# Performance work log

Hardware: AMD Instinct MI355X
Metric: run time of the kernel (lower is better)

The kernel has to match this reference:

```python
import jax, jax.numpy as jnp
import numpy as np

NEG_INF = -1e30

def setup_inputs() -> dict:
    key = jax.random.key(0)
    kC, kQ, kw = jax.random.split(key, 3)
    B, D, Lc, Lq = 32, 128, 2048, 64
    C = jax.random.normal(kC, (B, D, Lc), dtype=jnp.float32)
    Q = jax.random.normal(kQ, (B, D, Lq), dtype=jnp.float32)
    qmask = jnp.ones((B, Lq), dtype=jnp.float32)
    # trilinear weight, uniform(-sqrt(1/D), sqrt(1/D)) as in the torch init
    lim = (1.0 / D) ** 0.5
    w = jax.random.uniform(kw, (3 * D,), dtype=jnp.float32, minval=-lim, maxval=lim)
    return {"C": C, "Q": Q, "qmask": qmask, "w": w}

def reference(C, Q, qmask, w):
    # C: (B, D, Lc), Q: (B, D, Lq), qmask: (B, Lq), w: (3D,)
    Ct = jnp.transpose(C, (0, 2, 1))  # (B, Lc, D)
    Qt = jnp.transpose(Q, (0, 2, 1))  # (B, Lq, D)
    D = Ct.shape[-1]
    w1, w2, w3 = w[:D], w[D:2 * D], w[2 * D:]
    # trilinear similarity S[b,i,j] = Ct[b,i].w1 + Qt[b,j].w2 + (Ct[b,i]*Qt[b,j]).w3
    # computed WITHOUT the (B,Lc,Lq,3D) intermediate
    sc = Ct @ w1                                   # (B, Lc)
    sq = Qt @ w2                                   # (B, Lq)
    scq = jnp.einsum('bid,bjd->bij', Ct * w3, Qt)  # (B, Lc, Lq)
    S = sc[:, :, None] + sq[None if False else slice(None), None, :] + scq  # (B, Lc, Lq)
    m = qmask[:, None, :]                          # (B, 1, Lq)
    S1 = jax.nn.softmax(S * m + (1.0 - m) * NEG_INF, axis=2)  # over query axis
    S2 = jax.nn.softmax(S, axis=1)                             # over context axis
    A = jnp.einsum('bij,bjd->bid', S1, Qt)                     # (B, Lc, D)
    S1S2T = jnp.einsum('bij,bkj->bik', S1, S2)                 # (B, Lc, Lc) via S1 @ S2^T
    Bm = jnp.einsum('bik,bkd->bid', S1S2T, Ct)                 # (B, Lc, D)
    out = jnp.concatenate([Ct, A, Ct * A, Ct * Bm], axis=2)    # (B, Lc, 4D)
    # dropout is identity in eval mode
    return jnp.transpose(out, (0, 2, 1))                       # (B, 4D, Lc)
```

## Files before the change

### kernel.cpp

```cpp
#include <hip/hip_runtime.h>

#define LC 2048
#define DD 128
#define LQ 64
#define NPART 32
#define PADA 136
#define PADC 72

typedef unsigned short u16;
typedef unsigned int u32;
typedef __attribute__((ext_vector_type(8))) short bf16x8;
typedef __attribute__((ext_vector_type(4))) float f32x4;

__device__ inline u16 f2b(float f) {
  u32 u = __float_as_uint(f);
  u32 r = (u + 0x7fffu + ((u >> 16) & 1u)) >> 16;
  return (u16)r;
}
__device__ inline float b2f(u16 u) { return __uint_as_float(((u32)u) << 16); }
__device__ inline u32 pack2(float a, float b) {
  return (u32)f2b(a) | ((u32)f2b(b) << 16);
}

__global__ __launch_bounds__(256) void k13(const float* __restrict__ C,
                                           const float* __restrict__ Q,
                                           const float* __restrict__ w,
                                           const float* __restrict__ qmask,
                                           u16* __restrict__ S1g,
                                           float* __restrict__ Tu_part,
                                           float* __restrict__ Z_part, int B) {
  __shared__ u16 ldsA[128 * PADC];
  __shared__ u16 ldsB[64 * PADA];
  __shared__ float scp4[4][64], sqp4[4][64];
  __shared__ float scL[64], sqs[64], mkS[64], invL[64];
  int b = blockIdx.y, bx = blockIdx.x;
  int i0 = bx * 64, t = threadIdx.x;
  const float* Cb = C + (size_t)b * DD * LC;
  const float* Qb = Q + (size_t)b * DD * LQ;
  if (t < 64) mkS[t] = qmask[b * LQ + t];
  {
    int i = t & 63, dg = t >> 6;
    const float* Cp = Cb + i0 + i;
    float scp = 0.f;
#pragma unroll
    for (int dp = 0; dp < 16; ++dp) {
      int d = dg * 32 + 2 * dp;
      float c0 = Cp[(size_t)d * LC];
      float c1 = Cp[(size_t)(d + 1) * LC];
      scp = fmaf(c0, w[d], fmaf(c1, w[d + 1], scp));
      *(u32*)&ldsA[i * PADA + d] = pack2(c0, c1);
    }
    scp4[dg][i] = scp;
  }
  {
    int j = t & 63, dg = t >> 6;
    const float* Qp = Qb + j;
    float sqp = 0.f;
#pragma unroll
    for (int dp = 0; dp < 16; ++dp) {
      int d = dg * 32 + 2 * dp;
      float q0 = Qp[(size_t)d * LQ];
      float q1 = Qp[(size_t)(d + 1) * LQ];
      sqp = fmaf(q0, w[DD + d], fmaf(q1, w[DD + d + 1], sqp));
      *(u32*)&ldsB[j * PADA + d] = pack2(q0 * w[2 * DD + d], q1 * w[2 * DD + d + 1]);
    }
    sqp4[dg][j] = sqp;
  }
  __syncthreads();
  if (t < 64) scL[t] = scp4[0][t] + scp4[1][t] + scp4[2][t] + scp4[3][t];
  else if (t < 128) {
    int j = t - 64;
    sqs[j] = sqp4[0][j] + sqp4[1][j] + sqp4[2][j] + sqp4[3][j];
  }
  int lane = t & 63, wv = t >> 6;
  int lr = lane & 15, kg = lane >> 4;
  f32x4 acc[4];
#pragma unroll
  for (int nt = 0; nt < 4; ++nt) acc[nt] = (f32x4){0.f, 0.f, 0.f, 0.f};
#pragma unroll
  for (int ks = 0; ks < 4; ++ks) {
    bf16x8 af = *(bf16x8*)&ldsA[(wv * 16 + lr) * PADA + ks * 32 + kg * 8];
    bf16x8 bf[4];
#pragma unroll
    for (int nt = 0; nt < 4; ++nt)
      bf[nt] = *(bf16x8*)&ldsB[(nt * 16 + lr) * PADA + ks * 32 + kg * 8];
#pragma unroll
    for (int nt = 0; nt < 4; ++nt)
      acc[nt] = __builtin_amdgcn_mfma_f32_16x16x32_bf16(af, bf[nt], acc[nt], 0, 0, 0);
  }
  __syncthreads();
  {
    int ib = wv * 16 + kg * 4;
    float ev[4][4];
    float ps[4] = {0.f, 0.f, 0.f, 0.f};
#pragma unroll
    for (int nt = 0; nt < 4; ++nt) {
      int j = nt * 16 + lr;
      float sqv = sqs[j], mkv = mkS[j];
#pragma unroll
      for (int r = 0; r < 4; ++r) {
        float e = __expf(acc[nt][r] + scL[ib + r] + sqv);
        ev[nt][r] = e;
        ps[r] = fmaf(mkv, e, ps[r]);
      }
    }
#pragma unroll
    for (int r = 0; r < 4; ++r) {
      ps[r] += __shfl_xor(ps[r], 1, 64);
      ps[r] += __shfl_xor(ps[r], 2, 64);
      ps[r] += __shfl_xor(ps[r], 4, 64);
      ps[r] += __shfl_xor(ps[r], 8, 64);
    }
#pragma unroll
    for (int nt = 0; nt < 4; ++nt) {
      int j = nt * 16 + lr;
      u32 pk[2] = {pack2(ev[nt][0], ev[nt][1]), pack2(ev[nt][2], ev[nt][3])};
      *(uint2*)&ldsB[j * PADC + ib] = *(uint2*)pk;
    }
    if (lr == 0) {
#pragma unroll
      for (int r = 0; r < 4; ++r) invL[ib + r] = 1.f / fmaxf(ps[r], 1e-30f);
    }
  }
  {
    int d = t >> 1, half = t & 1;
    const float* src = Cb + (size_t)d * LC + i0 + half * 32;
#pragma unroll
    for (int ip = 0; ip < 8; ++ip) {
      float4 v = *(const float4*)&src[ip * 4];
      u32 pk[2] = {pack2(v.x, v.y), pack2(v.z, v.w)};
      *(uint2*)&ldsA[d * PADC + half * 32 + ip * 4] = *(uint2*)pk;
    }
  }
  __syncthreads();
  if (t < 64) {
    const u32* row = (const u32*)&ldsB[t * PADC];
    float z = 0.f;
#pragma unroll
    for (int q = 0; q < 32; ++q) {
      u32 v = row[q];
      z += b2f((u16)v) + b2f((u16)(v >> 16));
    }
    Z_part[((size_t)bx * B + b) * LQ + t] = z;
  }
  {
    int i = t >> 2, q4 = t & 3;
    float inv = invL[i];
    u32 opk[8];
#pragma unroll
    for (int q = 0; q < 8; ++q) {
      int j = q4 * 16 + 2 * q;
      float a0 = b2f(ldsB[j * PADC + i]) * mkS[j] * inv;
      float a1 = b2f(ldsB[(j + 1) * PADC + i]) * mkS[j + 1] * inv;
      opk[q] = pack2(a0, a1);
    }
    u16* dst = S1g + ((size_t)b * LC + i0 + i) * LQ + q4 * 16;
    *(uint4*)&dst[0] = *(uint4*)&opk[0];
    *(uint4*)&dst[8] = *(uint4*)&opk[4];
  }
  f32x4 tacc[2][4];
#pragma unroll
  for (int mt = 0; mt < 2; ++mt)
#pragma unroll
    for (int nt = 0; nt < 4; ++nt) tacc[mt][nt] = (f32x4){0.f, 0.f, 0.f, 0.f};
#pragma unroll
  for (int ks = 0; ks < 2; ++ks) {
    bf16x8 af[2], bf[4];
#pragma unroll
    for (int mt = 0; mt < 2; ++mt)
      af[mt] = *(bf16x8*)&ldsA[((wv * 2 + mt) * 16 + lr) * PADC + ks * 32 + kg * 8];
#pragma unroll
    for (int nt = 0; nt < 4; ++nt)
      bf[nt] = *(bf16x8*)&ldsB[(nt * 16 + lr) * PADC + ks * 32 + kg * 8];
#pragma unroll
    for (int mt = 0; mt < 2; ++mt)
#pragma unroll
      for (int nt = 0; nt < 4; ++nt)
        tacc[mt][nt] = __builtin_amdgcn_mfma_f32_16x16x32_bf16(af[mt], bf[nt],
                                                               tacc[mt][nt], 0, 0, 0);
  }
  float* Tp = Tu_part + ((size_t)bx * B + b) * LQ * DD;
#pragma unroll
  for (int mt = 0; mt < 2; ++mt)
#pragma unroll
    for (int nt = 0; nt < 4; ++nt) {
      int j = nt * 16 + lr;
      int db = (wv * 2 + mt) * 16 + kg * 4;
      *(f32x4*)&Tp[(size_t)j * DD + db] = tacc[mt][nt];
    }
}

__global__ __launch_bounds__(256) void k3b(const float* __restrict__ Tu_part,
                                           const float* __restrict__ Z_part,
                                           const float* __restrict__ Q,
                                           u16* __restrict__ TzT,
                                           u16* __restrict__ Qbf, int B) {
  __shared__ float Tsm[16][68];
  __shared__ float ziL[64];
  int b = blockIdx.y, d0 = blockIdx.x * 16;
  int t = threadIdx.x;
  {
    int dq = d0 + (t >> 4), jq = (t & 15) * 4;
    const float* qp = Q + ((size_t)b * DD + dq) * LQ + jq;
    u32 pk[2] = {pack2(qp[0], qp[1]), pack2(qp[2], qp[3])};
    *(uint2*)&Qbf[((size_t)b * DD + dq) * LQ + jq] = *(uint2*)pk;
  }
  int dd = t & 15, jg = t >> 4;
  float acc[4] = {};
#pragma unroll
  for (int p = 0; p < NPART; ++p) {
    const float* src = Tu_part + ((size_t)p * B + b) * LQ * DD + d0 + dd;
#pragma unroll
    for (int jj = 0; jj < 4; ++jj) acc[jj] += src[(jg * 4 + jj) * DD];
  }
  if (t < 64) {
    float z = 0.f;
#pragma unroll
    for (int p = 0; p < NPART; ++p) z += Z_part[((size_t)p * B + b) * LQ + t];
    ziL[t] = 1.f / z;
  }
  *(float4*)&Tsm[dd][jg * 4] = make_float4(acc[0], acc[1], acc[2], acc[3]);
  __syncthreads();
  if (t < 128) {
    int d = t >> 3, seg = t & 7;
    u32 pk[4];
#pragma unroll
    for (int q = 0; q < 4; ++q) {
      int j = seg * 8 + q * 2;
      pk[q] = pack2(Tsm[d][j] * ziL[j], Tsm[d][j + 1] * ziL[j + 1]);
    }
    *(uint4*)&TzT[((size_t)b * DD + d0 + d) * LQ + seg * 8] = *(uint4*)pk;
  }
}

__global__ __launch_bounds__(256) void k4(const u16* __restrict__ S1g,
                                          const u16* __restrict__ Qbf,
                                          const u16* __restrict__ TzT,
                                          const float* __restrict__ C,
                                          float* __restrict__ out) {
  int b = blockIdx.y, i0 = blockIdx.x * 64, t = threadIdx.x;
  int lane = t & 63, wv = t >> 6;
  int lr = lane & 15, kg = lane >> 4;
  bf16x8 Af[2];
  {
    size_t ri = ((size_t)b * LC + i0 + wv * 16 + lr) * LQ;
    Af[0] = *(const bf16x8*)&S1g[ri + kg * 8];
    Af[1] = *(const bf16x8*)&S1g[ri + 32 + kg * 8];
  }
  const u16* Qb = Qbf + (size_t)b * DD * LQ;
  const u16* Tzb = TzT + (size_t)b * DD * LQ;
  const float* Cb = C + (size_t)b * DD * LC + i0;
  float* outb = out + (size_t)b * 4 * DD * LC + i0;
  int irow = wv * 16 + kg * 4;
#pragma unroll
  for (int nt = 0; nt < 8; ++nt) {
    int d = nt * 16 + lr;
    bf16x8 QB[2], TB[2];
#pragma unroll
    for (int ks = 0; ks < 2; ++ks) {
      QB[ks] = *(const bf16x8*)&Qb[(size_t)d * LQ + ks * 32 + kg * 8];
      TB[ks] = *(const bf16x8*)&Tzb[(size_t)d * LQ + ks * 32 + kg * 8];
    }
    f32x4 accA = {0.f, 0.f, 0.f, 0.f}, accB = {0.f, 0.f, 0.f, 0.f};
    accA = __builtin_amdgcn_mfma_f32_16x16x32_bf16(Af[0], QB[0], accA, 0, 0, 0);
    accA = __builtin_amdgcn_mfma_f32_16x16x32_bf16(Af[1], QB[1], accA, 0, 0, 0);
    accB = __builtin_amdgcn_mfma_f32_16x16x32_bf16(Af[0], TB[0], accB, 0, 0, 0);
    accB = __builtin_amdgcn_mfma_f32_16x16x32_bf16(Af[1], TB[1], accB, 0, 0, 0);
    float4 c4 = *(const float4*)&Cb[(size_t)d * LC + irow];
    float4 oA = make_float4(accA[0], accA[1], accA[2], accA[3]);
    float4 oCA = make_float4(c4.x * accA[0], c4.y * accA[1], c4.z * accA[2],
                             c4.w * accA[3]);
    float4 oCB = make_float4(c4.x * accB[0], c4.y * accB[1], c4.z * accB[2],
                             c4.w * accB[3]);
    *(float4*)&outb[(size_t)d * LC + irow] = c4;
    *(float4*)&outb[(size_t)(DD + d) * LC + irow] = oA;
    *(float4*)&outb[(size_t)(2 * DD + d) * LC + irow] = oCA;
    *(float4*)&outb[(size_t)(3 * DD + d) * LC + irow] = oCB;
  }
}

extern "C" void kernel_launch(void* const* d_in, const int* in_sizes, int n_in,
                              void* d_out, int out_size, void* d_ws, size_t ws_size,
                              hipStream_t stream) {
  const float* C = (const float*)d_in[0];
  const float* Q = (const float*)d_in[1];
  const float* qmask = (const float*)d_in[2];
  const float* w = (const float*)d_in[3];
  float* out = (float*)d_out;
  int B = in_sizes[2] / LQ;

  char* p = (char*)d_ws;
  u16* S1g = (u16*)p;           p += (size_t)B * LC * LQ * 2;
  u16* TzT = (u16*)p;           p += (size_t)B * DD * LQ * 2;
  u16* Qbf = (u16*)p;           p += (size_t)B * DD * LQ * 2;
  float* Tu_part = (float*)p;   p += (size_t)NPART * B * LQ * DD * 4;
  float* Z_part = (float*)p;

  k13<<<dim3(LC / 64, B), 256, 0, stream>>>(C, Q, w, qmask, S1g, Tu_part, Z_part, B);
  k3b<<<dim3(DD / 16, B), 256, 0, stream>>>(Tu_part, Z_part, Q, TzT, Qbf, B);
  k4<<<dim3(LC / 64, B), 256, 0, stream>>>(S1g, Qbf, TzT, C, out);
}
```

Baseline: 77.70 us.

## Precompute weighted bf16 Q once per batch in a new prologue kernel

```diff
diff --git a/kernel.cpp b/kernel.cpp
--- a/kernel.cpp
+++ b/kernel.cpp
@@ -4,8 +4,6 @@
 #define DD 128
 #define LQ 64
 #define NPART 32
-#define PADA 136
-#define PADC 72
 
 typedef unsigned short u16;
 typedef unsigned int u32;
@@ -22,56 +20,102 @@
   return (u32)f2b(a) | ((u32)f2b(b) << 16);
 }
 
+__global__ __launch_bounds__(256) void kq(const float* __restrict__ Q,
+                                          const float* __restrict__ w,
+                                          u16* __restrict__ Qwg,
+                                          float* __restrict__ sqg,
+                                          u16* __restrict__ Qbf) {
+  __shared__ float qs[128][65];
+  __shared__ float red[4][64];
+  int b = blockIdx.x, t = threadIdx.x;
+  const float* Qb = Q + (size_t)b * DD * LQ;
+  {
+    int base = t * 32;
+#pragma unroll
+    for (int q = 0; q < 8; ++q) {
+      float4 v = *(const float4*)&Qb[base + q * 4];
+      int k = base + q * 4;
+      int d = k >> 6, j = k & 63;
+      qs[d][j] = v.x; qs[d][j + 1] = v.y; qs[d][j + 2] = v.z; qs[d][j + 3] = v.w;
+    }
+  }
+  __syncthreads();
+  {
+    int j = t & 63, dq = t >> 6;
+    float sqp = 0.f;
+    u32 pk[16];
+#pragma unroll
+    for (int dp = 0; dp < 16; ++dp) {
+      int d = dq * 32 + 2 * dp;
+      float q0 = qs[d][j], q1 = qs[d + 1][j];
+      sqp = fmaf(q0, w[DD + d], fmaf(q1, w[DD + d + 1], sqp));
+      pk[dp] = pack2(q0 * w[2 * DD + d], q1 * w[2 * DD + d + 1]);
+    }
+    u16* dst = Qwg + ((size_t)b * LQ + j) * DD + dq * 32;
+#pragma unroll
+    for (int q = 0; q < 4; ++q) *(uint4*)&dst[q * 8] = *(uint4*)&pk[q * 4];
+    red[dq][j] = sqp;
+  }
+  {
+    int d = t >> 1, half = t & 1;
+    u32 pk[16];
+#pragma unroll
+    for (int q = 0; q < 16; ++q)
+      pk[q] = pack2(qs[d][half * 32 + 2 * q], qs[d][half * 32 + 2 * q + 1]);
+    u16* dst = Qbf + ((size_t)b * DD + d) * LQ + half * 32;
+#pragma unroll
+    for (int q = 0; q < 4; ++q) *(uint4*)&dst[q * 8] = *(uint4*)&pk[q * 4];
+  }
+  __syncthreads();
+  if (t < 64) sqg[b * LQ + t] = red[0][t] + red[1][t] + red[2][t] + red[3][t];
+}
+
 __global__ __launch_bounds__(256) void k13(const float* __restrict__ C,
-                                           const float* __restrict__ Q,
+                                           const u16* __restrict__ Qwg,
+                                           const float* __restrict__ sqg,
+                                           const float* __restrict__ qmask,
                                            const float* __restrict__ w,
-                                           const float* __restrict__ qmask,
                                            u16* __restrict__ S1g,
                                            float* __restrict__ Tu_part,
                                            float* __restrict__ Z_part, int B) {
-  __shared__ u16 ldsA[128 * PADC];
-  __shared__ u16 ldsB[64 * PADA];
-  __shared__ float scp4[4][64], sqp4[4][64];
+  __shared__ u16 ldsA[128 * 72];
+  __shared__ u16 ldsB[64 * 136];
+  __shared__ float scp4[4][64];
   __shared__ float scL[64], sqs[64], mkS[64], invL[64];
   int b = blockIdx.y, bx = blockIdx.x;
   int i0 = bx * 64, t = threadIdx.x;
   const float* Cb = C + (size_t)b * DD * LC;
-  const float* Qb = Q + (size_t)b * DD * LQ;
-  if (t < 64) mkS[t] = qmask[b * LQ + t];
   {
     int i = t & 63, dg = t >> 6;
     const float* Cp = Cb + i0 + i;
     float scp = 0.f;
+    u32 pk[16];
 #pragma unroll
     for (int dp = 0; dp < 16; ++dp) {
       int d = dg * 32 + 2 * dp;
       float c0 = Cp[(size_t)d * LC];
       float c1 = Cp[(size_t)(d + 1) * LC];
       scp = fmaf(c0, w[d], fmaf(c1, w[d + 1], scp));
-      *(u32*)&ldsA[i * PADA + d] = pack2(c0, c1);
-    }
+      pk[dp] = pack2(c0, c1);
+    }
+#pragma unroll
+    for (int q = 0; q < 4; ++q)
+      *(uint4*)&ldsA[i * 136 + dg * 32 + q * 8] = *(uint4*)&pk[q * 4];
     scp4[dg][i] = scp;
   }
   {
-    int j = t & 63, dg = t >> 6;
-    const float* Qp = Qb + j;
-    float sqp = 0.f;
-#pragma unroll
-    for (int dp = 0; dp < 16; ++dp) {
-      int d = dg * 32 + 2 * dp;
-      float q0 = Qp[(size_t)d * LQ];
-      float q1 = Qp[(size_t)(d + 1) * LQ];
-      sqp = fmaf(q0, w[DD + d], fmaf(q1, w[DD + d + 1], sqp));
-      *(u32*)&ldsB[j * PADA + d] = pack2(q0 * w[2 * DD + d], q1 * w[2 * DD + d + 1]);
-    }
-    sqp4[dg][j] = sqp;
+    int row = t & 63, quarter = t >> 6;
+    const u16* src = Qwg + ((size_t)b * LQ + row) * DD + quarter * 32;
+#pragma unroll
+    for (int q = 0; q < 4; ++q)
+      *(uint4*)&ldsB[row * 136 + quarter * 32 + q * 8] = *(const uint4*)&src[q * 8];
+  }
+  if (t < 64) {
+    sqs[t] = sqg[b * LQ + t];
+    mkS[t] = qmask[b * LQ + t];
   }
   __syncthreads();
   if (t < 64) scL[t] = scp4[0][t] + scp4[1][t] + scp4[2][t] + scp4[3][t];
-  else if (t < 128) {
-    int j = t - 64;
-    sqs[j] = sqp4[0][j] + sqp4[1][j] + sqp4[2][j] + sqp4[3][j];
-  }
   int lane = t & 63, wv = t >> 6;
   int lr = lane & 15, kg = lane >> 4;
   f32x4 acc[4];
@@ -79,11 +123,11 @@
   for (int nt = 0; nt < 4; ++nt) acc[nt] = (f32x4){0.f, 0.f, 0.f, 0.f};
 #pragma unroll
   for (int ks = 0; ks < 4; ++ks) {
-    bf16x8 af = *(bf16x8*)&ldsA[(wv * 16 + lr) * PADA + ks * 32 + kg * 8];
+    bf16x8 af = *(bf16x8*)&ldsA[(wv * 16 + lr) * 136 + ks * 32 + kg * 8];
     bf16x8 bf[4];
 #pragma unroll
     for (int nt = 0; nt < 4; ++nt)
-      bf[nt] = *(bf16x8*)&ldsB[(nt * 16 + lr) * PADA + ks * 32 + kg * 8];
+      bf[nt] = *(bf16x8*)&ldsB[(nt * 16 + lr) * 136 + ks * 32 + kg * 8];
 #pragma unroll
     for (int nt = 0; nt < 4; ++nt)
       acc[nt] = __builtin_amdgcn_mfma_f32_16x16x32_bf16(af, bf[nt], acc[nt], 0, 0, 0);
@@ -115,7 +159,7 @@
     for (int nt = 0; nt < 4; ++nt) {
       int j = nt * 16 + lr;
       u32 pk[2] = {pack2(ev[nt][0], ev[nt][1]), pack2(ev[nt][2], ev[nt][3])};
-      *(uint2*)&ldsB[j * PADC + ib] = *(uint2*)pk;
+      *(uint2*)&ldsB[j * 72 + ib] = *(uint2*)pk;
     }
     if (lr == 0) {
 #pragma unroll
@@ -125,16 +169,20 @@
   {
     int d = t >> 1, half = t & 1;
     const float* src = Cb + (size_t)d * LC + i0 + half * 32;
+    u32 pk[16];
 #pragma unroll
     for (int ip = 0; ip < 8; ++ip) {
       float4 v = *(const float4*)&src[ip * 4];
-      u32 pk[2] = {pack2(v.x, v.y), pack2(v.z, v.w)};
-      *(uint2*)&ldsA[d * PADC + half * 32 + ip * 4] = *(uint2*)pk;
-    }
+      pk[2 * ip] = pack2(v.x, v.y);
+      pk[2 * ip + 1] = pack2(v.z, v.w);
+    }
+#pragma unroll
+    for (int q = 0; q < 4; ++q)
+      *(uint4*)&ldsA[d * 72 + half * 32 + q * 8] = *(uint4*)&pk[q * 4];
   }
   __syncthreads();
   if (t < 64) {
-    const u32* row = (const u32*)&ldsB[t * PADC];
+    const u32* row = (const u32*)&ldsB[t * 72];
     float z = 0.f;
 #pragma unroll
     for (int q = 0; q < 32; ++q) {
@@ -150,8 +198,8 @@
 #pragma unroll
     for (int q = 0; q < 8; ++q) {
       int j = q4 * 16 + 2 * q;
-      float a0 = b2f(ldsB[j * PADC + i]) * mkS[j] * inv;
-      float a1 = b2f(ldsB[(j + 1) * PADC + i]) * mkS[j + 1] * inv;
+      float a0 = b2f(ldsB[j * 72 + i]) * mkS[j] * inv;
+      float a1 = b2f(ldsB[(j + 1) * 72 + i]) * mkS[j + 1] * inv;
       opk[q] = pack2(a0, a1);
     }
     u16* dst = S1g + ((size_t)b * LC + i0 + i) * LQ + q4 * 16;
@@ -168,10 +216,10 @@
     bf16x8 af[2], bf[4];
 #pragma unroll
     for (int mt = 0; mt < 2; ++mt)
-      af[mt] = *(bf16x8*)&ldsA[((wv * 2 + mt) * 16 + lr) * PADC + ks * 32 + kg * 8];
+      af[mt] = *(bf16x8*)&ldsA[((wv * 2 + mt) * 16 + lr) * 72 + ks * 32 + kg * 8];
 #pragma unroll
     for (int nt = 0; nt < 4; ++nt)
-      bf[nt] = *(bf16x8*)&ldsB[(nt * 16 + lr) * PADC + ks * 32 + kg * 8];
+      bf[nt] = *(bf16x8*)&ldsB[(nt * 16 + lr) * 72 + ks * 32 + kg * 8];
 #pragma unroll
     for (int mt = 0; mt < 2; ++mt)
 #pragma unroll
@@ -192,26 +240,19 @@
 
 __global__ __launch_bounds__(256) void k3b(const float* __restrict__ Tu_part,
                                            const float* __restrict__ Z_part,
-                                           const float* __restrict__ Q,
-                                           u16* __restrict__ TzT,
-                                           u16* __restrict__ Qbf, int B) {
+                                           u16* __restrict__ TzT, int B) {
   __shared__ float Tsm[16][68];
   __shared__ float ziL[64];
   int b = blockIdx.y, d0 = blockIdx.x * 16;
   int t = threadIdx.x;
   {
-    int dq = d0 + (t >> 4), jq = (t & 15) * 4;
-    const float* qp = Q + ((size_t)b * DD + dq) * LQ + jq;
-    u32 pk[2] = {pack2(qp[0], qp[1]), pack2(qp[2], qp[3])};
-    *(uint2*)&Qbf[((size_t)b * DD + dq) * LQ + jq] = *(uint2*)pk;
-  }
-  int dd = t & 15, jg = t >> 4;
-  float acc[4] = {};
-#pragma unroll
-  for (int p = 0; p < NPART; ++p) {
-    const float* src = Tu_part + ((size_t)p * B + b) * LQ * DD + d0 + dd;
-#pragma unroll
-    for (int jj = 0; jj < 4; ++jj) acc[jj] += src[(jg * 4 + jj) * DD];
+    int j = t >> 2, dseg = t & 3;
+    f32x4 acc = {0.f, 0.f, 0.f, 0.f};
+#pragma unroll
+    for (int p = 0; p < NPART; ++p)
+      acc += *(const f32x4*)&Tu_part[((size_t)p * B + b) * LQ * DD + (size_t)j * DD + d0 + dseg * 4];
+#pragma unroll
+    for (int r = 0; r < 4; ++r) Tsm[dseg * 4 + r][j] = acc[r];
   }
   if (t < 64) {
     float z = 0.f;
@@ -219,7 +260,6 @@
     for (int p = 0; p < NPART; ++p) z += Z_part[((size_t)p * B + b) * LQ + t];
     ziL[t] = 1.f / z;
   }
-  *(float4*)&Tsm[dd][jg * 4] = make_float4(acc[0], acc[1], acc[2], acc[3]);
   __syncthreads();
   if (t < 128) {
     int d = t >> 3, seg = t & 7;
@@ -293,10 +333,13 @@
   u16* S1g = (u16*)p;           p += (size_t)B * LC * LQ * 2;
   u16* TzT = (u16*)p;           p += (size_t)B * DD * LQ * 2;
   u16* Qbf = (u16*)p;           p += (size_t)B * DD * LQ * 2;
+  u16* Qwg = (u16*)p;           p += (size_t)B * LQ * DD * 2;
   float* Tu_part = (float*)p;   p += (size_t)NPART * B * LQ * DD * 4;
-  float* Z_part = (float*)p;
-
-  k13<<<dim3(LC / 64, B), 256, 0, stream>>>(C, Q, w, qmask, S1g, Tu_part, Z_part, B);
-  k3b<<<dim3(DD / 16, B), 256, 0, stream>>>(Tu_part, Z_part, Q, TzT, Qbf, B);
+  float* Z_part = (float*)p;    p += (size_t)NPART * B * LQ * 4;
+  float* sqg = (float*)p;
+
+  kq<<<B, 256, 0, stream>>>(Q, w, Qwg, sqg, Qbf);
+  k13<<<dim3(LC / 64, B), 256, 0, stream>>>(C, Qwg, sqg, qmask, w, S1g, Tu_part, Z_part, B);
+  k3b<<<dim3(DD / 16, B), 256, 0, stream>>>(Tu_part, Z_part, TzT, B);
   k4<<<dim3(LC / 64, B), 256, 0, stream>>>(S1g, Qbf, TzT, C, out);
 }
```

After: 74.60 us. -4.0%, faster.
